# Performance work log

Hardware: AMD Instinct MI355X
Metric: run time of the kernel (lower is better)

The kernel has to match this reference:

```python
import jax, jax.numpy as jnp
import numpy as np

B, T, D_IN, D_OUT, H = 4, 2048, 768, 768, 12
HD = D_OUT // H  # 64


def setup_inputs() -> dict:
    key = jax.random.key(0)
    ks = jax.random.split(key, 6)
    s_in = 1.0 / np.sqrt(D_IN)
    s_out = 1.0 / np.sqrt(D_OUT)
    return {
        "x": jax.random.normal(ks[0], (B, T, D_IN), dtype=jnp.float32),
        "Wq": jax.random.uniform(ks[1], (D_IN, D_OUT), jnp.float32, -s_in, s_in),
        "Wk": jax.random.uniform(ks[2], (D_IN, D_OUT), jnp.float32, -s_in, s_in),
        "Wv": jax.random.uniform(ks[3], (D_IN, D_OUT), jnp.float32, -s_in, s_in),
        "Wo": jax.random.uniform(ks[4], (D_OUT, D_OUT), jnp.float32, -s_out, s_out),
        "bo": jax.random.uniform(ks[5], (D_OUT,), jnp.float32, -s_out, s_out),
    }


def reference(x, Wq, Wk, Wv, Wo, bo):
    b, t, _ = x.shape
    # QKV projections (no bias, per qkv_bias=False), split into heads: [b,h,t,hd]
    q = (x @ Wq).reshape(b, t, H, HD).transpose(0, 2, 1, 3)
    k = (x @ Wk).reshape(b, t, H, HD).transpose(0, 2, 1, 3)
    v = (x @ Wv).reshape(b, t, H, HD).transpose(0, 2, 1, 3)
    # NOTE: original calls masked_fill (non-in-place) and discards the result,
    # so NO causal mask is actually applied. Faithfully reproduce that.
    scores = jnp.einsum("bhqd,bhkd->bhqk", q, k)  # [b,h,t,t]
    attn = jax.nn.softmax(scores / jnp.sqrt(jnp.float32(HD)), axis=-1)
    # dropout p=0.0 (eval) -> identity
    ctx = jnp.einsum("bhqk,bhkd->bhqd", attn, v)  # [b,h,t,hd]
    ctx = ctx.transpose(0, 2, 1, 3).reshape(b, t, D_OUT)
    return ctx @ Wo + bo
```

## Files before the change

kernel.cpp:

```cpp
#include <hip/hip_runtime.h>
#include <hip/hip_bf16.h>
#include <stdint.h>


#define HH   12
#define TT   2048
#define DIN  768
#define DOUT 768
#define HD   64
#define BB   4
#define MTOT (BB*TT)
#define NQKV (3*DOUT)
#define QSCALE 0.1803368801111832f

typedef float  float4v __attribute__((ext_vector_type(4)));
typedef __bf16 bf16x8  __attribute__((ext_vector_type(8)));
typedef short  short8v __attribute__((ext_vector_type(8)));

#define AS1 __attribute__((address_space(1)))
#define AS3 __attribute__((address_space(3)))

static __device__ __forceinline__ void gload_lds16(const void* g, void* l) {
    __builtin_amdgcn_global_load_lds((AS1 void*)g, (AS3 void*)l, 16, 0, 0);
}

static __device__ __forceinline__ short f2bf(float f) {
    __bf16 h = (__bf16)f;
    return __builtin_bit_cast(short, h);
}

__global__ __launch_bounds__(256) void cast_x_kernel(const float* __restrict__ x,
                                                     short* __restrict__ xb, int n4) {
    int i = blockIdx.x * 256 + threadIdx.x;
    if (i >= n4) return;
    float4 v = ((const float4*)x)[i];
    short4 o;
    o.x = f2bf(v.x); o.y = f2bf(v.y); o.z = f2bf(v.z); o.w = f2bf(v.w);
    ((short4*)xb)[i] = o;
}

__global__ __launch_bounds__(256) void prep_w_kernel(const float* __restrict__ Wq,
                                                     const float* __restrict__ Wk,
                                                     const float* __restrict__ Wv,
                                                     const float* __restrict__ Wo,
                                                     short* __restrict__ Wqkvt,
                                                     short* __restrict__ Wot) {
    __shared__ short tile[32 * 33];
    const int bx = blockIdx.x, by = blockIdx.y, bz = blockIdx.z;
    const float* W = (bz == 0) ? Wq : (bz == 1) ? Wk : (bz == 2) ? Wv : Wo;
    const int tx = threadIdx.x & 31, ty = threadIdx.x >> 5;
    for (int i = 0; i < 4; i++) {
        int k = by * 32 + ty + i * 8;
        tile[(ty + i * 8) * 33 + tx] = f2bf(W[(size_t)k * DOUT + bx * 32 + tx]);
    }
    __syncthreads();
    for (int i = 0; i < 4; i++) {
        int n = bx * 32 + ty + i * 8;
        int k = by * 32 + tx;
        short v = tile[tx * 33 + ty + i * 8];
        if (bz < 3) Wqkvt[(size_t)(bz * DOUT + n) * DIN + k] = v;
        else        Wot[(size_t)n * DOUT + k] = v;
    }
}

__global__ __launch_bounds__(256) void qkv_gemm_kernel(const short* __restrict__ Xb,
                                                       const short* __restrict__ Wt,
                                                       short* __restrict__ Qb,
                                                       short* __restrict__ Kb,
                                                       short* __restrict__ Vt) {
    __shared__ __align__(16) short ldsA[128 * 32];
    __shared__ __align__(16) short ldsB[128 * 32];
    const int t = threadIdx.x;
    const int w = t >> 6, lane = t & 63;
    const int quad = lane >> 4, l15 = lane & 15;
    const int m0 = blockIdx.x * 128, n0 = blockIdx.y * 128;
    const int wm = (w >> 1) * 64, wn = (w & 1) * 64;

    float4v acc[4][4];
    for (int i = 0; i < 4; i++)
        for (int j = 0; j < 4; j++)
            acc[i][j] = (float4v)0.0f;

    const int rA = t >> 2;
    const int cSw = ((t & 3) ^ ((t >> 3) & 3)) * 8;
    const short* gA0 = Xb + (size_t)(m0 + rA) * DIN + cSw;
    const short* gB0 = Wt + (size_t)(n0 + rA) * DIN + cSw;
    const int pos = (quad ^ ((l15 >> 1) & 3)) * 8;

    for (int k0 = 0; k0 < DIN; k0 += 32) {
        gload_lds16(gA0 + k0,            &ldsA[t * 8]);
        gload_lds16(gA0 + 64 * DIN + k0, &ldsA[(t + 256) * 8]);
        gload_lds16(gB0 + k0,            &ldsB[t * 8]);
        gload_lds16(gB0 + 64 * DIN + k0, &ldsB[(t + 256) * 8]);
        __syncthreads();
        bf16x8 af[4], bfr[4];
        for (int i = 0; i < 4; i++) af[i]  = *(const bf16x8*)&ldsA[(wm + i * 16 + l15) * 32 + pos];
        for (int j = 0; j < 4; j++) bfr[j] = *(const bf16x8*)&ldsB[(wn + j * 16 + l15) * 32 + pos];
        for (int i = 0; i < 4; i++)
            for (int j = 0; j < 4; j++)
                acc[i][j] = __builtin_amdgcn_mfma_f32_16x16x32_bf16(af[i], bfr[j], acc[i][j], 0, 0, 0);
        __syncthreads();
    }

    const int which = n0 / DOUT;
    if (which < 2) {
        for (int i = 0; i < 4; i++) {
            int m = m0 + wm + i * 16 + quad * 4;
            int b = m >> 11, tq = m & 2047;
            for (int j = 0; j < 4; j++) {
                int n = n0 + wn + j * 16 + l15;
                int col = n - which * DOUT;
                int hh = col >> 6, d = col & 63;
                for (int r = 0; r < 4; r++) {
                    float v = acc[i][j][r];
                    if (which == 0)
                        Qb[((size_t)((b * HH + hh) * TT + tq + r) << 6) + d] = f2bf(v * QSCALE);
                    else
                        Kb[((size_t)((b * HH + hh) * TT + tq + r) << 6) + d] = f2bf(v);
                }
            }
        }
    } else {
        short* ldsT = ldsA;
        const int n0r = n0 - 2 * DOUT;
        const int b = m0 >> 11, tq0 = m0 & 2047;
        for (int mh = 0; mh < 2; mh++) {
            __syncthreads();
            if ((w >> 1) == mh) {
                for (int i = 0; i < 4; i++)
                    for (int j = 0; j < 4; j++)
                        for (int r = 0; r < 4; r++) {
                            int nl = wn + j * 16 + l15;
                            int ml = i * 16 + quad * 4 + r;
                            int c = ml >> 3, o = ml & 7;
                            ldsT[nl * 64 + ((c ^ (nl & 7)) * 8 + o)] = f2bf(acc[i][j][r]);
                        }
            }
            __syncthreads();
            for (int pass = 0; pass < 4; pass++) {
                int nrow = pass * 32 + (t >> 3);
                int cc = t & 7;
                short8v v = *(const short8v*)&ldsT[nrow * 64 + ((cc ^ (nrow & 7)) * 8)];
                int colg = n0r + nrow;
                int hh = colg >> 6, d = colg & 63;
                *(short8v*)&Vt[(size_t)((b * HH + hh) * HD + d) * TT + tq0 + mh * 64 + cc * 8] = v;
            }
        }
    }
}

__global__ __launch_bounds__(256, 4) void attn_kernel(const short* __restrict__ Qb,
                                                      const short* __restrict__ Kb,
                                                      const short* __restrict__ Vt,
                                                      short* __restrict__ Ctx) {
    __shared__ __align__(16) short ldsK[2][64 * 64];
    __shared__ __align__(16) short ldsV[2][64 * 64];
    __shared__ __align__(16) short ldsP[4][16 * 64];
    const int t = threadIdx.x;
    const int w = t >> 6, lane = t & 63;
    const int quad = lane >> 4, l15 = lane & 15;
    const int bh = blockIdx.x;
    const int b = bh / HH, h = bh - b * HH;
    const int q0 = blockIdx.y * 128 + w * 32;

    const short* Qbase = Qb + (size_t)bh * TT * HD;
    const short* Kbase = Kb + (size_t)bh * TT * HD;
    const short* Vbase = Vt + (size_t)bh * HD * TT;

    bf16x8 aq[2][2];
#pragma unroll
    for (int tile = 0; tile < 2; tile++)
#pragma unroll
        for (int f = 0; f < 2; f++)
            aq[tile][f] = *(const bf16x8*)&Qbase[(q0 + tile * 16 + l15) * HD + f * 32 + quad * 8];

    float lsum[2] = {0.0f, 0.0f};
    float4v accO[2][4];
#pragma unroll
    for (int tile = 0; tile < 2; tile++)
#pragma unroll
        for (int j = 0; j < 4; j++) accO[tile][j] = (float4v)0.0f;

    const int rS = t >> 3;
    const int cS8 = ((t & 7) ^ ((t >> 3) & 7)) * 8;
    const int rpos = l15 & 7;

    auto stage = [&](int buf, int u0) {
        gload_lds16(Kbase + (size_t)(u0 + rS) * HD + cS8,      &ldsK[buf][t * 8]);
        gload_lds16(Kbase + (size_t)(u0 + rS + 32) * HD + cS8, &ldsK[buf][(t + 256) * 8]);
        gload_lds16(Vbase + (size_t)rS * TT + u0 + cS8,        &ldsV[buf][t * 8]);
        gload_lds16(Vbase + (size_t)(rS + 32) * TT + u0 + cS8, &ldsV[buf][(t + 256) * 8]);
    };

    stage(0, 0);

    short* Pw = (short*)&ldsP[w][0];

    for (int it = 0; it < TT / 64; ++it) {
        __syncthreads();
        const int buf = it & 1;
        if (it + 1 < TT / 64) stage(buf ^ 1, (it + 1) * 64);
        const short* K_ = &ldsK[buf][0];
        const short* V_ = &ldsV[buf][0];

#pragma unroll
        for (int tile = 0; tile < 2; tile++) {
            float4v st[4];
#pragma unroll
            for (int jj = 0; jj < 4; jj++) st[jj] = (float4v)0.0f;
#pragma unroll
            for (int f = 0; f < 2; f++) {
#pragma unroll
                for (int jj = 0; jj < 4; jj++) {
                    bf16x8 bk = *(const bf16x8*)&K_[(jj * 16 + l15) * 64 + (((f * 4 + quad) ^ rpos) * 8)];
                    st[jj] = __builtin_amdgcn_mfma_f32_16x16x32_bf16(bk, aq[tile][f], st[jj], 0, 0, 0);
                }
            }
#pragma unroll
            for (int jj = 0; jj < 4; jj++) {
                float p0 = __builtin_amdgcn_exp2f(st[jj][0]);
                float p1 = __builtin_amdgcn_exp2f(st[jj][1]);
                float p2 = __builtin_amdgcn_exp2f(st[jj][2]);
                float p3 = __builtin_amdgcn_exp2f(st[jj][3]);
                lsum[tile] += (p0 + p1) + (p2 + p3);
                short4 s4;
                s4.x = f2bf(p0); s4.y = f2bf(p1); s4.z = f2bf(p2); s4.w = f2bf(p3);
                int cw = jj * 2 + (quad >> 1);
                *(short4*)&Pw[l15 * 64 + ((cw ^ rpos) * 8 + (quad & 1) * 4)] = s4;
            }
#pragma unroll
            for (int f = 0; f < 2; f++) {
                bf16x8 ap = *(const bf16x8*)&Pw[l15 * 64 + (((f * 4 + quad) ^ rpos) * 8)];
#pragma unroll
                for (int j = 0; j < 4; j++) {
                    bf16x8 bv = *(const bf16x8*)&V_[(j * 16 + l15) * 64 + (((f * 4 + quad) ^ rpos) * 8)];
                    accO[tile][j] = __builtin_amdgcn_mfma_f32_16x16x32_bf16(ap, bv, accO[tile][j], 0, 0, 0);
                }
            }
        }
    }

    float lrow[2][4];
#pragma unroll
    for (int tile = 0; tile < 2; tile++) {
        float v = lsum[tile];
        v += __shfl_xor(v, 16);
        v += __shfl_xor(v, 32);
        float linv = 1.0f / v;
#pragma unroll
        for (int r = 0; r < 4; r++)
            lrow[tile][r] = __shfl(linv, (lane & 48) + quad * 4 + r);
    }

#pragma unroll
    for (int tile = 0; tile < 2; tile++)
#pragma unroll
        for (int j = 0; j < 4; j++)
#pragma unroll
            for (int r = 0; r < 4; r++) {
                int qg = q0 + tile * 16 + quad * 4 + r;
                Ctx[(size_t)(b * TT + qg) * DOUT + h * HD + j * 16 + l15] =
                    f2bf(accO[tile][j][r] * lrow[tile][r]);
            }
}

__global__ __launch_bounds__(256) void out_gemm_kernel(const short* __restrict__ Cb,
                                                       const short* __restrict__ Wot,
                                                       const float* __restrict__ bo,
                                                       float* __restrict__ out) {
    __shared__ __align__(16) short ldsA[128 * 32];
    __shared__ __align__(16) short ldsB[128 * 32];
    const int t = threadIdx.x;
    const int w = t >> 6, lane = t & 63;
    const int quad = lane >> 4, l15 = lane & 15;
    const int m0 = blockIdx.x * 128, n0 = blockIdx.y * 128;
    const int wm = (w >> 1) * 64, wn = (w & 1) * 64;

    float4v acc[4][4];
    for (int i = 0; i < 4; i++)
        for (int j = 0; j < 4; j++)
            acc[i][j] = (float4v)0.0f;

    const int rA = t >> 2;
    const int cSw = ((t & 3) ^ ((t >> 3) & 3)) * 8;
    const short* gA0 = Cb + (size_t)(m0 + rA) * DOUT + cSw;
    const short* gB0 = Wot + (size_t)(n0 + rA) * DOUT + cSw;
    const int pos = (quad ^ ((l15 >> 1) & 3)) * 8;

    for (int k0 = 0; k0 < DOUT; k0 += 32) {
        gload_lds16(gA0 + k0,             &ldsA[t * 8]);
        gload_lds16(gA0 + 64 * DOUT + k0, &ldsA[(t + 256) * 8]);
        gload_lds16(gB0 + k0,             &ldsB[t * 8]);
        gload_lds16(gB0 + 64 * DOUT + k0, &ldsB[(t + 256) * 8]);
        __syncthreads();
        bf16x8 af[4], bfr[4];
        for (int i = 0; i < 4; i++) af[i]  = *(const bf16x8*)&ldsA[(wm + i * 16 + l15) * 32 + pos];
        for (int j = 0; j < 4; j++) bfr[j] = *(const bf16x8*)&ldsB[(wn + j * 16 + l15) * 32 + pos];
        for (int i = 0; i < 4; i++)
            for (int j = 0; j < 4; j++)
                acc[i][j] = __builtin_amdgcn_mfma_f32_16x16x32_bf16(af[i], bfr[j], acc[i][j], 0, 0, 0);
        __syncthreads();
    }

    for (int i = 0; i < 4; i++) {
        int m = m0 + wm + i * 16 + quad * 4;
        for (int j = 0; j < 4; j++) {
            int n = n0 + wn + j * 16 + l15;
            float bias = bo[n];
            for (int r = 0; r < 4; r++)
                out[(size_t)(m + r) * DOUT + n] = acc[i][j][r] + bias;
        }
    }
}

extern "C" void kernel_launch(void* const* d_in, const int* in_sizes, int n_in,
                              void* d_out, int out_size, void* d_ws, size_t ws_size,
                              hipStream_t stream) {
    const float* x  = (const float*)d_in[0];
    const float* Wq = (const float*)d_in[1];
    const float* Wk = (const float*)d_in[2];
    const float* Wv = (const float*)d_in[3];
    const float* Wo = (const float*)d_in[4];
    const float* bo = (const float*)d_in[5];
    float* out = (float*)d_out;

    char* ws = (char*)d_ws;
    short* Xb    = (short*)(ws + 0);
    short* Wqkvt = (short*)(ws + 12582912);
    short* Wot   = (short*)(ws + 16121856);
    short* Qb    = (short*)(ws + 17301504);
    short* Kb    = (short*)(ws + 29884416);
    short* Vt    = (short*)(ws + 42467328);
    short* Cb    = (short*)(ws + 55050240);

    cast_x_kernel<<<(MTOT * DIN / 4 + 255) / 256, 256, 0, stream>>>(x, Xb, MTOT * DIN / 4);
    prep_w_kernel<<<dim3(24, 24, 4), 256, 0, stream>>>(Wq, Wk, Wv, Wo, Wqkvt, Wot);
    qkv_gemm_kernel<<<dim3(MTOT / 128, NQKV / 128), 256, 0, stream>>>(Xb, Wqkvt, Qb, Kb, Vt);
    attn_kernel<<<dim3(BB * HH, TT / 128), 256, 0, stream>>>(Qb, Kb, Vt, Cb);
    out_gemm_kernel<<<dim3(MTOT / 128, DOUT / 128), 256, 0, stream>>>(Cb, Wot, bo, out);
}
```

Baseline: 221.9 us.

## Use 32x32 MFMA in attention with register-resident P and LDS-staged Q/K stores

The attention kernel moves from 16x16x32 to 32x32x16 bf16 MFMA. Each wave now covers 64 queries, and the block shrinks to 128 threads. K rows are permuted at load time so the exp'd score accumulator maps straight onto the A-operand layout of the PV MFMA, which removes the LDS round-trip for P. The QKV GEMM epilogue for Q and K now transposes through LDS to issue 16-byte coalesced stores instead of scattered 2-byte stores. The trade-off is more accumulator registers per wave and possibly lower occupancy in the attention kernel.

```diff
diff --git a/kernel.cpp b/kernel.cpp
--- a/kernel.cpp
+++ b/kernel.cpp
@@ -13,9 +13,10 @@
 #define NQKV (3*DOUT)
 #define QSCALE 0.1803368801111832f
 
-typedef float  float4v __attribute__((ext_vector_type(4)));
-typedef __bf16 bf16x8  __attribute__((ext_vector_type(8)));
-typedef short  short8v __attribute__((ext_vector_type(8)));
+typedef float  float4v  __attribute__((ext_vector_type(4)));
+typedef float  float16v __attribute__((ext_vector_type(16)));
+typedef __bf16 bf16x8   __attribute__((ext_vector_type(8)));
+typedef short  short8v  __attribute__((ext_vector_type(8)));
 
 #define AS1 __attribute__((address_space(1)))
 #define AS3 __attribute__((address_space(3)))
@@ -68,8 +69,9 @@
                                                        short* __restrict__ Qb,
                                                        short* __restrict__ Kb,
                                                        short* __restrict__ Vt) {
-    __shared__ __align__(16) short ldsA[128 * 32];
-    __shared__ __align__(16) short ldsB[128 * 32];
+    __shared__ __align__(16) short lds[8192];
+    short* ldsA = lds;
+    short* ldsB = lds + 4096;
     const int t = threadIdx.x;
     const int w = t >> 6, lane = t & 63;
     const int quad = lane >> 4, l15 = lane & 15;
@@ -104,28 +106,40 @@
 
     const int which = n0 / DOUT;
     if (which < 2) {
-        for (int i = 0; i < 4; i++) {
-            int m = m0 + wm + i * 16 + quad * 4;
-            int b = m >> 11, tq = m & 2047;
-            for (int j = 0; j < 4; j++) {
-                int n = n0 + wn + j * 16 + l15;
-                int col = n - which * DOUT;
-                int hh = col >> 6, d = col & 63;
-                for (int r = 0; r < 4; r++) {
-                    float v = acc[i][j][r];
-                    if (which == 0)
-                        Qb[((size_t)((b * HH + hh) * TT + tq + r) << 6) + d] = f2bf(v * QSCALE);
-                    else
-                        Kb[((size_t)((b * HH + hh) * TT + tq + r) << 6) + d] = f2bf(v);
-                }
-            }
+        short* ldsT = lds;
+        const float sc = (which == 0) ? QSCALE : 1.0f;
+        short* dst = (which == 0) ? Qb : Kb;
+        const int n0sec = n0 - which * DOUT;
+        for (int mh = 0; mh < 2; mh++) {
+            if ((w >> 1) == mh) {
+                for (int i = 0; i < 4; i++)
+                    for (int j = 0; j < 4; j++) {
+                        int col = wn + j * 16 + l15;
+                        int cx = col >> 3, co = col & 7;
+                        for (int r = 0; r < 4; r++) {
+                            int row = i * 16 + quad * 4 + r;
+                            ldsT[row * 128 + ((cx ^ (row & 7)) * 8 + co)] = f2bf(acc[i][j][r] * sc);
+                        }
+                    }
+            }
+            __syncthreads();
+            for (int p = 0; p < 4; p++) {
+                int row = p * 16 + (t >> 4);
+                int cL = t & 15;
+                short8v v = *(const short8v*)&ldsT[row * 128 + ((cL ^ (row & 7)) * 8)];
+                int mg = m0 + mh * 64 + row;
+                int b2 = mg >> 11, tq = mg & 2047;
+                int colg = n0sec + cL * 8;
+                int hh = colg >> 6, d = colg & 63;
+                *(short8v*)&dst[((size_t)((b2 * HH + hh) * TT + tq) << 6) + d] = v;
+            }
+            __syncthreads();
         }
     } else {
-        short* ldsT = ldsA;
+        short* ldsT = lds;
         const int n0r = n0 - 2 * DOUT;
         const int b = m0 >> 11, tq0 = m0 & 2047;
         for (int mh = 0; mh < 2; mh++) {
-            __syncthreads();
             if ((w >> 1) == mh) {
                 for (int i = 0; i < 4; i++)
                     for (int j = 0; j < 4; j++)
@@ -145,56 +159,61 @@
                 int hh = colg >> 6, d = colg & 63;
                 *(short8v*)&Vt[(size_t)((b * HH + hh) * HD + d) * TT + tq0 + mh * 64 + cc * 8] = v;
             }
+            __syncthreads();
         }
     }
 }
 
-__global__ __launch_bounds__(256, 4) void attn_kernel(const short* __restrict__ Qb,
+__global__ __launch_bounds__(128, 2) void attn_kernel(const short* __restrict__ Qb,
                                                       const short* __restrict__ Kb,
                                                       const short* __restrict__ Vt,
                                                       short* __restrict__ Ctx) {
     __shared__ __align__(16) short ldsK[2][64 * 64];
     __shared__ __align__(16) short ldsV[2][64 * 64];
-    __shared__ __align__(16) short ldsP[4][16 * 64];
     const int t = threadIdx.x;
     const int w = t >> 6, lane = t & 63;
-    const int quad = lane >> 4, l15 = lane & 15;
+    const int half = lane >> 5, m = lane & 31;
     const int bh = blockIdx.x;
     const int b = bh / HH, h = bh - b * HH;
-    const int q0 = blockIdx.y * 128 + w * 32;
+    const int q0 = blockIdx.y * 128 + w * 64;
 
     const short* Qbase = Qb + (size_t)bh * TT * HD;
     const short* Kbase = Kb + (size_t)bh * TT * HD;
     const short* Vbase = Vt + (size_t)bh * HD * TT;
 
-    bf16x8 aq[2][2];
+    bf16x8 qf[2][4];
 #pragma unroll
     for (int tile = 0; tile < 2; tile++)
 #pragma unroll
-        for (int f = 0; f < 2; f++)
-            aq[tile][f] = *(const bf16x8*)&Qbase[(q0 + tile * 16 + l15) * HD + f * 32 + quad * 8];
-
+        for (int s = 0; s < 4; s++)
+            qf[tile][s] = *(const bf16x8*)&Qbase[(q0 + tile * 32 + m) * HD + s * 16 + half * 8];
+
+    int kOff[4], vOff[4], dOff[4];
+#pragma unroll
+    for (int g = 0; g < 4; g++) {
+        int row = g * 16 + (t >> 3);
+        int r5 = row & 31, kt = row >> 5;
+        int pi = ((r5 >> 3) & 1) * 16 + ((r5 >> 2) & 1) * 8 + ((r5 >> 4) & 1) * 4 + (r5 & 3);
+        kOff[g] = (kt * 32 + pi) * 64 + (((t & 7) ^ (row & 7)) * 8);
+        vOff[g] = row * TT + (((t & 7) ^ (row & 7)) * 8);
+        dOff[g] = (g * 128 + t) * 8;
+    }
+
+    auto stage = [&](int buf, int u0) {
+#pragma unroll
+        for (int g = 0; g < 4; g++)
+            gload_lds16(Kbase + (size_t)u0 * 64 + kOff[g], &ldsK[buf][dOff[g]]);
+#pragma unroll
+        for (int g = 0; g < 4; g++)
+            gload_lds16(Vbase + (size_t)u0 + vOff[g], &ldsV[buf][dOff[g]]);
+    };
+
+    float16v accO[2][2];
+    accO[0][0] = (float16v)0.0f; accO[0][1] = (float16v)0.0f;
+    accO[1][0] = (float16v)0.0f; accO[1][1] = (float16v)0.0f;
     float lsum[2] = {0.0f, 0.0f};
-    float4v accO[2][4];
-#pragma unroll
-    for (int tile = 0; tile < 2; tile++)
-#pragma unroll
-        for (int j = 0; j < 4; j++) accO[tile][j] = (float4v)0.0f;
-
-    const int rS = t >> 3;
-    const int cS8 = ((t & 7) ^ ((t >> 3) & 7)) * 8;
-    const int rpos = l15 & 7;
-
-    auto stage = [&](int buf, int u0) {
-        gload_lds16(Kbase + (size_t)(u0 + rS) * HD + cS8,      &ldsK[buf][t * 8]);
-        gload_lds16(Kbase + (size_t)(u0 + rS + 32) * HD + cS8, &ldsK[buf][(t + 256) * 8]);
-        gload_lds16(Vbase + (size_t)rS * TT + u0 + cS8,        &ldsV[buf][t * 8]);
-        gload_lds16(Vbase + (size_t)(rS + 32) * TT + u0 + cS8, &ldsV[buf][(t + 256) * 8]);
-    };
 
     stage(0, 0);
-
-    short* Pw = (short*)&ldsP[w][0];
 
     for (int it = 0; it < TT / 64; ++it) {
         __syncthreads();
@@ -204,64 +223,62 @@
         const short* V_ = &ldsV[buf][0];
 
 #pragma unroll
-        for (int tile = 0; tile < 2; tile++) {
-            float4v st[4];
-#pragma unroll
-            for (int jj = 0; jj < 4; jj++) st[jj] = (float4v)0.0f;
-#pragma unroll
-            for (int f = 0; f < 2; f++) {
-#pragma unroll
-                for (int jj = 0; jj < 4; jj++) {
-                    bf16x8 bk = *(const bf16x8*)&K_[(jj * 16 + l15) * 64 + (((f * 4 + quad) ^ rpos) * 8)];
-                    st[jj] = __builtin_amdgcn_mfma_f32_16x16x32_bf16(bk, aq[tile][f], st[jj], 0, 0, 0);
+        for (int kt = 0; kt < 2; kt++) {
+            float16v st[2];
+            st[0] = (float16v)0.0f; st[1] = (float16v)0.0f;
+#pragma unroll
+            for (int s = 0; s < 4; s++) {
+                bf16x8 ka = *(const bf16x8*)&K_[(kt * 32 + m) * 64 + (((s * 2 + half) ^ (m & 7)) * 8)];
+                st[0] = __builtin_amdgcn_mfma_f32_32x32x16_bf16(ka, qf[0][s], st[0], 0, 0, 0);
+                st[1] = __builtin_amdgcn_mfma_f32_32x32x16_bf16(ka, qf[1][s], st[1], 0, 0, 0);
+            }
+            bf16x8 ap[2][2];
+#pragma unroll
+            for (int tile = 0; tile < 2; tile++) {
+                float pe[16];
+#pragma unroll
+                for (int i = 0; i < 16; i++) pe[i] = __builtin_amdgcn_exp2f(st[tile][i]);
+                float s01 = 0.0f;
+#pragma unroll
+                for (int i = 0; i < 16; i++) s01 += pe[i];
+                lsum[tile] += s01;
+#pragma unroll
+                for (int i = 0; i < 4; i++) {
+                    ap[tile][0][i]     = (__bf16)pe[i];
+                    ap[tile][0][4 + i] = (__bf16)pe[8 + i];
+                    ap[tile][1][i]     = (__bf16)pe[4 + i];
+                    ap[tile][1][4 + i] = (__bf16)pe[12 + i];
                 }
             }
 #pragma unroll
-            for (int jj = 0; jj < 4; jj++) {
-                float p0 = __builtin_amdgcn_exp2f(st[jj][0]);
-                float p1 = __builtin_amdgcn_exp2f(st[jj][1]);
-                float p2 = __builtin_amdgcn_exp2f(st[jj][2]);
-                float p3 = __builtin_amdgcn_exp2f(st[jj][3]);
-                lsum[tile] += (p0 + p1) + (p2 + p3);
-                short4 s4;
-                s4.x = f2bf(p0); s4.y = f2bf(p1); s4.z = f2bf(p2); s4.w = f2bf(p3);
-                int cw = jj * 2 + (quad >> 1);
-                *(short4*)&Pw[l15 * 64 + ((cw ^ rpos) * 8 + (quad & 1) * 4)] = s4;
-            }
-#pragma unroll
-            for (int f = 0; f < 2; f++) {
-                bf16x8 ap = *(const bf16x8*)&Pw[l15 * 64 + (((f * 4 + quad) ^ rpos) * 8)];
-#pragma unroll
-                for (int j = 0; j < 4; j++) {
-                    bf16x8 bv = *(const bf16x8*)&V_[(j * 16 + l15) * 64 + (((f * 4 + quad) ^ rpos) * 8)];
-                    accO[tile][j] = __builtin_amdgcn_mfma_f32_16x16x32_bf16(ap, bv, accO[tile][j], 0, 0, 0);
+            for (int ks = 0; ks < 2; ks++)
+#pragma unroll
+                for (int dt = 0; dt < 2; dt++) {
+                    int row = dt * 32 + m;
+                    bf16x8 bv = *(const bf16x8*)&V_[row * 64 + (((kt * 4 + ks * 2 + half) ^ (row & 7)) * 8)];
+                    accO[0][dt] = __builtin_amdgcn_mfma_f32_32x32x16_bf16(ap[0][ks], bv, accO[0][dt], 0, 0, 0);
+                    accO[1][dt] = __builtin_amdgcn_mfma_f32_32x32x16_bf16(ap[1][ks], bv, accO[1][dt], 0, 0, 0);
                 }
-            }
         }
     }
 
-    float lrow[2][4];
 #pragma unroll
     for (int tile = 0; tile < 2; tile++) {
-        float v = lsum[tile];
-        v += __shfl_xor(v, 16);
-        v += __shfl_xor(v, 32);
+        float v = lsum[tile] + __shfl_xor(lsum[tile], 32);
         float linv = 1.0f / v;
 #pragma unroll
-        for (int r = 0; r < 4; r++)
-            lrow[tile][r] = __shfl(linv, (lane & 48) + quad * 4 + r);
-    }
-
-#pragma unroll
-    for (int tile = 0; tile < 2; tile++)
-#pragma unroll
-        for (int j = 0; j < 4; j++)
-#pragma unroll
-            for (int r = 0; r < 4; r++) {
-                int qg = q0 + tile * 16 + quad * 4 + r;
-                Ctx[(size_t)(b * TT + qg) * DOUT + h * HD + j * 16 + l15] =
-                    f2bf(accO[tile][j][r] * lrow[tile][r]);
-            }
+        for (int s = 0; s < 4; s++)
+#pragma unroll
+            for (int i = 0; i < 4; i++) {
+                int reg = s * 4 + i;
+                int qrow = i + s * 8 + half * 4;
+                float ln = __shfl(linv, qrow);
+                int qg = q0 + tile * 32 + qrow;
+                size_t base = (size_t)(b * TT + qg) * DOUT + h * HD + m;
+                Ctx[base]      = f2bf(accO[tile][0][reg] * ln);
+                Ctx[base + 32] = f2bf(accO[tile][1][reg] * ln);
+            }
+    }
 }
 
 __global__ __launch_bounds__(256) void out_gemm_kernel(const short* __restrict__ Cb,
@@ -336,6 +353,6 @@
     cast_x_kernel<<<(MTOT * DIN / 4 + 255) / 256, 256, 0, stream>>>(x, Xb, MTOT * DIN / 4);
     prep_w_kernel<<<dim3(24, 24, 4), 256, 0, stream>>>(Wq, Wk, Wv, Wo, Wqkvt, Wot);
     qkv_gemm_kernel<<<dim3(MTOT / 128, NQKV / 128), 256, 0, stream>>>(Xb, Wqkvt, Qb, Kb, Vt);
-    attn_kernel<<<dim3(BB * HH, TT / 128), 256, 0, stream>>>(Qb, Kb, Vt, Cb);
+    attn_kernel<<<dim3(BB * HH, TT / 128), 128, 0, stream>>>(Qb, Kb, Vt, Cb);
     out_gemm_kernel<<<dim3(MTOT / 128, DOUT / 128), 256, 0, stream>>>(Cb, Wot, bo, out);
 }
```

Result: no change. 222.4 us (+0.2%).
